# Kernel optimization log

Hardware: AMD Instinct MI355X
Metric: run time of the kernel (lower is better)

Reference implementation:

```python
import jax, jax.numpy as jnp
import numpy as np

N, E, IN, H, C, ED = 50000, 400000, 128, 8, 32, 16
NEG = 0.2   # LeakyReLU negative_slope
EPS = 1e-5  # LayerNorm eps


def _glorot(k, fan_in, fan_out, shape=None):
    lim = float(np.sqrt(6.0 / (fan_in + fan_out)))
    shape = (fan_in, fan_out) if shape is None else shape
    return jax.random.uniform(k, shape, jnp.float32, -lim, lim)


def setup_inputs() -> dict:
    key = jax.random.key(0)
    ks = jax.random.split(key, 16)
    x = jax.random.normal(ks[0], (N, IN), jnp.float32)
    src = jax.random.randint(ks[1], (E,), 0, N, jnp.int32)
    off = jax.random.randint(ks[2], (E,), 1, N, jnp.int32)
    dst = ((src + off) % N).astype(jnp.int32)  # guarantees no self loops
    edge_index = jnp.stack([src, dst])
    edge_attr = jax.random.normal(ks[3], (E, ED), jnp.float32) * 0.5
    d = {"x": x, "edge_index": edge_index, "edge_attr": edge_attr}
    i = 4
    for l, cin in [(1, IN), (2, C)]:
        d[f"Wl{l}"] = _glorot(ks[i], cin, H * C); i += 1
        d[f"bl{l}"] = jnp.zeros((H * C,), jnp.float32)
        d[f"Wr{l}"] = _glorot(ks[i], cin, H * C); i += 1
        d[f"br{l}"] = jnp.zeros((H * C,), jnp.float32)
        d[f"We{l}"] = _glorot(ks[i], ED, H * C); i += 1  # lin_edge, bias=False
        d[f"att{l}"] = _glorot(ks[i], H * C, 1, shape=(H, C)); i += 1
        d[f"bias{l}"] = jnp.zeros((C,), jnp.float32)
    d["ln_g"] = jnp.ones((C,), jnp.float32)
    d["ln_b"] = jnp.zeros((C,), jnp.float32)
    return d


def _seg_softmax(e, idx, n):
    # softmax over edges grouped by destination node (variable-degree neighborhoods)
    m = jax.ops.segment_max(e, idx, num_segments=n)
    p = jnp.exp(e - m[idx])
    s = jax.ops.segment_sum(p, idx, num_segments=n)
    return p / (s[idx] + 1e-16)


def _gat_layer(xx, src, dst, ea, Wl, bl, Wr, br, We, att, bias):
    n = xx.shape[0]
    xl = (xx @ Wl + bl).reshape(n, H, C)   # source transform (also the message)
    xr = (xx @ Wr + br).reshape(n, H, C)   # target transform
    ee = (ea @ We).reshape(-1, H, C)       # edge transform
    z = jax.nn.leaky_relu(xl[src] + xr[dst] + ee, NEG)      # [E', H, C]
    logits = jnp.einsum('ehc,hc->eh', z, att)               # [E', H]
    alpha = _seg_softmax(logits, dst, n)
    out = jax.ops.segment_sum(alpha[:, :, None] * xl[src], dst, num_segments=n)
    return out.mean(axis=1) + bias  # concat=False -> mean over heads


def _layernorm(xx, g, b):
    mu = jnp.mean(xx, -1, keepdims=True)
    var = jnp.mean((xx - mu) ** 2, -1, keepdims=True)
    return (xx - mu) * jax.lax.rsqrt(var + EPS) * g + b


def reference(x, edge_index, edge_attr, Wl1, bl1, Wr1, br1, We1, att1, bias1, ln_g, ln_b, Wl2, bl2, Wr2, br2, We2, att2, bias2):
    src, dst = edge_index[0], edge_index[1]
    # add_self_loops with fill_value='mean': self-loop attr = mean of incoming edge attrs
    deg = jax.ops.segment_sum(jnp.ones((E,), jnp.float32), dst, num_segments=N)
    loop_attr = jax.ops.segment_sum(edge_attr, dst, num_segments=N) / jnp.maximum(deg, 1.0)[:, None]
    ar = jnp.arange(N, dtype=src.dtype)
    src_f = jnp.concatenate([src, ar])
    dst_f = jnp.concatenate([dst, ar])
    ea_f = jnp.concatenate([edge_attr, loop_attr], axis=0)
    h = _gat_layer(x, src_f, dst_f, ea_f, Wl1, bl1, Wr1, br1, We1, att1, bias1)
    h = _layernorm(jax.nn.relu(h), ln_g, ln_b)
    h = _gat_layer(h, src_f, dst_f, ea_f, Wl2, bl2, Wr2, br2, We2, att2, bias2)
    return h
```

## Files before the change

### kernel.cpp

```cpp
#include <hip/hip_runtime.h>
#include <hip/hip_bf16.h>

#define N_NODES 50000
#define N_EDGES 400000
#define EP (N_EDGES + N_NODES)
#define IN_F 128
#define H_HEADS 8
#define C_CH 32
#define HC 256
#define ED_F 16
#define NEG_SLOPE 0.2f
#define LN_EPS 1e-5f
#define NB_SCAN ((N_NODES + 2047) / 2048)
#define NDBINS 1024
#define KF_NB 2048

typedef __hip_bfloat16 bf16;
typedef float v2f __attribute__((ext_vector_type(2)));
typedef short bf16x8 __attribute__((ext_vector_type(8)));
typedef float f32x4 __attribute__((ext_vector_type(4)));

__device__ __forceinline__ float bfu(unsigned short v){
    return __uint_as_float((unsigned int)v << 16);
}
__device__ __forceinline__ unsigned short f2b(float v){
    bf16 t = __float2bfloat16(v);
    return *reinterpret_cast<unsigned short*>(&t);
}

#define CASTX_NB 3125
#define W1_NB 128
#define W2_NB 32

__device__ __forceinline__ void prepW_body(const float* __restrict__ W,
                                           unsigned short* __restrict__ Wt,
                                           int K, int idx){
    if (idx >= 256 * K) return;
    int c = idx & 255, k = idx >> 8;
    Wt[(size_t)c * K + k] = f2b(W[idx]);
}

__global__ void k_prep(const float* __restrict__ x, unsigned short* __restrict__ xb,
                       const float* __restrict__ Wl1, unsigned short* __restrict__ Wt1l,
                       const float* __restrict__ Wr1, unsigned short* __restrict__ Wt1r,
                       const float* __restrict__ Wl2, unsigned short* __restrict__ Wt2l,
                       const float* __restrict__ Wr2, unsigned short* __restrict__ Wt2r){
    int b = blockIdx.x, t = threadIdx.x;
    if (b < CASTX_NB){
        int i = b * 256 + t;
        if (i >= N_NODES * IN_F / 8) return;
        const float4* p = reinterpret_cast<const float4*>(x + (size_t)i * 8);
        float4 v0 = p[0], v1 = p[1];
        unsigned short o[8] = {f2b(v0.x), f2b(v0.y), f2b(v0.z), f2b(v0.w),
                               f2b(v1.x), f2b(v1.y), f2b(v1.z), f2b(v1.w)};
        *reinterpret_cast<uint4*>(xb + (size_t)i * 8) = *reinterpret_cast<uint4*>(o);
    } else if (b < CASTX_NB + W1_NB){
        prepW_body(Wl1, Wt1l, IN_F, (b - CASTX_NB) * 256 + t);
    } else if (b < CASTX_NB + 2 * W1_NB){
        prepW_body(Wr1, Wt1r, IN_F, (b - CASTX_NB - W1_NB) * 256 + t);
    } else if (b < CASTX_NB + 2 * W1_NB + W2_NB){
        prepW_body(Wl2, Wt2l, C_CH, (b - CASTX_NB - 2 * W1_NB) * 256 + t);
    } else {
        prepW_body(Wr2, Wt2r, C_CH, (b - CASTX_NB - 2 * W1_NB - W2_NB) * 256 + t);
    }
}


__global__ void k_deg(const int* __restrict__ dstA, int* __restrict__ deg){
    int e = blockIdx.x * 256 + threadIdx.x;
    if (e < N_EDGES) atomicAdd(&deg[dstA[e]], 1);
}

__global__ void k_scanA(const int* __restrict__ deg, int* __restrict__ ptr,
                        int* __restrict__ bsum){
    __shared__ int wsum[4];
    int blk = blockIdx.x;
    int base0 = blk * 2048;
    int t = threadIdx.x, lane = t & 63, wv = t >> 6;
    int carry = 0;
    for (int c = 0; c < 8; ++c){
        int i = base0 + c * 256 + t;
        int v = (i < N_NODES) ? (deg[i] + 1) : 0;
        int x = v;
#pragma unroll
        for (int off = 1; off < 64; off <<= 1){
            int y = __shfl_up(x, off, 64);
            if (lane >= off) x += y;
        }
        if (lane == 63) wsum[wv] = x;
        __syncthreads();
        int pre = carry;
        for (int j = 0; j < wv; ++j) pre += wsum[j];
        if (i < N_NODES) ptr[i] = pre + x - v;
        int tot = wsum[0] + wsum[1] + wsum[2] + wsum[3];
        __syncthreads();
        carry += tot;
    }
    if (t == 0) bsum[blk] = carry;
}

__global__ void k_scanB(const int* __restrict__ bsum, int* __restrict__ boff){
    int t = threadIdx.x;
    int v = (t < NB_SCAN) ? bsum[t] : 0;
    int x = v;
#pragma unroll
    for (int off = 1; off < 64; off <<= 1){
        int y = __shfl_up(x, off, 64);
        if (t >= off) x += y;
    }
    if (t < NB_SCAN) boff[t] = x - v;
    if (t == 63) boff[NB_SCAN] = x;
}

__global__ void k_scanC(int* __restrict__ ptr, const int* __restrict__ boff){
    int i = blockIdx.x * 256 + threadIdx.x;
    if (i < N_NODES) ptr[i] += boff[i >> 11];
    else if (i == N_NODES) ptr[i] = boff[NB_SCAN];
}

__global__ void k_scatter(const int* __restrict__ dstA, const int* __restrict__ ptr,
                          int* __restrict__ cur, int* __restrict__ eid){
    int e = blockIdx.x * 256 + threadIdx.x;
    if (e >= EP) return;
    int n = (e < N_EDGES) ? dstA[e] : (e - N_EDGES);
    int p = ptr[n] + atomicAdd(&cur[n], 1);
    eid[p] = e;
}

__global__ void k_sort(const int* __restrict__ ptr, int* __restrict__ eid,
                       const int* __restrict__ srcA, int2* __restrict__ es){
    int n = blockIdx.x * 256 + threadIdx.x;
    if (n >= N_NODES) return;
    int b = ptr[n], t = ptr[n + 1];
    for (int i = b + 1; i < t; ++i){
        int v = eid[i]; int j = i - 1;
        while (j >= b && eid[j] > v){ eid[j + 1] = eid[j]; --j; }
        eid[j + 1] = v;
    }
    for (int i = b; i < t; ++i){
        int e = eid[i];
        es[i] = make_int2(e, (e < N_EDGES) ? srcA[e] : n);
    }
}

__global__ void k_loopattr(const int* __restrict__ ptr, const int* __restrict__ eid,
                           const float* __restrict__ ea, const int* __restrict__ deg,
                           float* __restrict__ la){
    int idx = blockIdx.x * 256 + threadIdx.x;
    if (idx >= N_NODES * ED_F) return;
    int n = idx >> 4, j = idx & 15;
    float s = 0.f;
    int b = ptr[n], t = ptr[n + 1];
    for (int i = b; i < t; ++i){
        int e = eid[i];
        if (e < N_EDGES) s += ea[(size_t)e * ED_F + j];
    }
    la[idx] = s / (float)max(deg[n], 1);
}

__global__ void k_hist(const int* __restrict__ ptr, int* __restrict__ hist){
    __shared__ int lh[NDBINS];
    int t = threadIdx.x;
    for (int i = t; i < NDBINS; i += 256) lh[i] = 0;
    __syncthreads();
    int n = blockIdx.x * 256 + t;
    if (n < N_NODES){
        int d = min(ptr[n + 1] - ptr[n], NDBINS - 1);
        atomicAdd(&lh[NDBINS - 1 - d], 1);
    }
    __syncthreads();
    for (int i = t; i < NDBINS; i += 256)
        if (lh[i]) atomicAdd(&hist[i], lh[i]);
}

__global__ void k_scanH(const int* __restrict__ hist, int* __restrict__ hoff){
    __shared__ int wsum[4];
    __shared__ int carry_s;
    int t = threadIdx.x, lane = t & 63, wv = t >> 6;
    if (t == 0) carry_s = 0;
    __syncthreads();
    for (int base = 0; base < NDBINS; base += 256){
        int i = base + t;
        int v = hist[i];
        int x = v;
#pragma unroll
        for (int off = 1; off < 64; off <<= 1){
            int y = __shfl_up(x, off, 64);
            if (lane >= off) x += y;
        }
        if (lane == 63) wsum[wv] = x;
        __syncthreads();
        int pre = carry_s;
        for (int j = 0; j < wv; ++j) pre += wsum[j];
        hoff[i] = pre + x - v;
        int tot = wsum[0] + wsum[1] + wsum[2] + wsum[3];
        __syncthreads();
        if (t == 0) carry_s += tot;
        __syncthreads();
    }
}

__global__ void k_place(const int* __restrict__ ptr, const int* __restrict__ hoff,
                        int* __restrict__ hcur, int* __restrict__ ord){
    __shared__ int lh[NDBINS];
    __shared__ int lbase[NDBINS];
    int t = threadIdx.x;
    for (int i = t; i < NDBINS; i += 256) lh[i] = 0;
    __syncthreads();
    int n = blockIdx.x * 256 + t;
    int b = -1, lr = 0;
    if (n < N_NODES){
        int d = min(ptr[n + 1] - ptr[n], NDBINS - 1);
        b = NDBINS - 1 - d;
        lr = atomicAdd(&lh[b], 1);
    }
    __syncthreads();
    for (int i = t; i < NDBINS; i += 256)
        if (lh[i]) lbase[i] = atomicAdd(&hcur[i], lh[i]);
    __syncthreads();
    if (n < N_NODES) ord[hoff[b] + lbase[b] + lr] = n;
}

template<int K>
__global__ __launch_bounds__(256)
void k_gemmM(const unsigned short* __restrict__ A,
             const unsigned short* __restrict__ Wtl, const float* __restrict__ bl,
             const unsigned short* __restrict__ Wtr, const float* __restrict__ br,
             bf16* __restrict__ xlh, unsigned short* __restrict__ xrh){
    const int cb = blockIdx.y;
    const unsigned short* Wt = (cb < 2) ? Wtl : Wtr;
    const float* bs = (cb < 2) ? bl : br;
    const int c0 = (cb & 1) * 128;
    const int r0 = blockIdx.x * 64;

    __shared__ unsigned short sA[64][40];
    __shared__ unsigned short sW[128][40];

    const int tid = threadIdx.x;
    const int lane = tid & 63;
    const int w = tid >> 6;

    f32x4 acc[8] = {};

    for (int kt = 0; kt < K; kt += 32){
        {
            int row = tid >> 2, kc = (tid & 3) * 8;
            int gr = r0 + row;
            uint4 v = make_uint4(0, 0, 0, 0);
            if (gr < N_NODES)
                v = *reinterpret_cast<const uint4*>(&A[(size_t)gr * K + kt + kc]);
            *reinterpret_cast<uint4*>(&sA[row][kc]) = v;
        }
        {
            int c = tid >> 1, kc = (tid & 1) * 16;
            const unsigned short* src = &Wt[(size_t)(c0 + c) * K + kt + kc];
            *reinterpret_cast<uint4*>(&sW[c][kc])     = *reinterpret_cast<const uint4*>(src);
            *reinterpret_cast<uint4*>(&sW[c][kc + 8]) = *reinterpret_cast<const uint4*>(src + 8);
        }
        __syncthreads();
        int kchunk = (lane >> 4) * 8;
        bf16x8 af = *reinterpret_cast<const bf16x8*>(&sA[w * 16 + (lane & 15)][kchunk]);
#pragma unroll
        for (int f = 0; f < 8; ++f){
            bf16x8 bfr = *reinterpret_cast<const bf16x8*>(&sW[f * 16 + (lane & 15)][kchunk]);
            acc[f] = __builtin_amdgcn_mfma_f32_16x16x32_bf16(af, bfr, acc[f], 0, 0, 0);
        }
        __syncthreads();
    }
    int colL = lane & 15;
    int rbase = (lane >> 4) * 4;
#pragma unroll
    for (int f = 0; f < 8; ++f){
        int col = c0 + f * 16 + colL;
        float bv = bs[col];
#pragma unroll
        for (int r = 0; r < 4; ++r){
            int gr = r0 + w * 16 + rbase + r;
            if (gr < N_NODES){
                float ov = acc[f][r] + bv;
                if (cb < 2) xlh[(size_t)gr * HC + col] = __float2bfloat16(ov);
                else        xrh[(size_t)gr * HC + col] = f2b(ov);
            }
        }
    }
}

template<int MODE>
__global__ __launch_bounds__(256)
__attribute__((amdgpu_waves_per_eu(3, 4)))
void k_fused(const bf16* __restrict__ xlh, const unsigned short* __restrict__ xrh,
             const float* __restrict__ ea, const float* __restrict__ la,
             const int2* __restrict__ es, const int* __restrict__ ptr,
             const int* __restrict__ ord,
             const float* __restrict__ We, const float* __restrict__ att,
             const float* __restrict__ bias, const float* __restrict__ lng,
             const float* __restrict__ lnb,
             unsigned short* __restrict__ h1b, float* __restrict__ outF){
    const int wv = threadIdx.x >> 6;
    const int lane = threadIdx.x & 63;
    const int c0 = lane * 4;
    const int k = lane & 7;

    v2f we2[ED_F][2];
#pragma unroll
    for (int j = 0; j < ED_F; ++j){
        float4 t4 = *reinterpret_cast<const float4*>(We + (size_t)j * HC + c0);
        we2[j][0] = v2f{t4.x, t4.y};
        we2[j][1] = v2f{t4.z, t4.w};
    }
    float4 at4 = *reinterpret_cast<const float4*>(att + c0);
    float attr[4] = {at4.x, at4.y, at4.z, at4.w};

#define EDGE_MLP(PK, AR, AK)                                              \
        {                                                                 \
            v2f z[2] = {AK[0] + xrv[0], AK[1] + xrv[1]};                  \
            _Pragma("unroll")                                             \
            for (int j4 = 0; j4 < 4; ++j4){                               \
                float4 e4 = *reinterpret_cast<const float4*>(AR + j4 * 4);\
                const float ej[4] = {e4.x, e4.y, e4.z, e4.w};             \
                _Pragma("unroll")                                         \
                for (int jj = 0; jj < 4; ++jj){                           \
                    int j = j4 * 4 + jj;                                  \
                    v2f ejv = {ej[jj], ej[jj]};                           \
                    z[0] += ejv * we2[j][0];                              \
                    z[1] += ejv * we2[j][1];                              \
                }                                                         \
            }                                                             \
            float zz0 = z[0].x, zz1 = z[0].y, zz2 = z[1].x, zz3 = z[1].y; \
            zz0 = (zz0 < 0.f) ? NEG_SLOPE * zz0 : zz0;                    \
            zz1 = (zz1 < 0.f) ? NEG_SLOPE * zz1 : zz1;                    \
            zz2 = (zz2 < 0.f) ? NEG_SLOPE * zz2 : zz2;                    \
            zz3 = (zz3 < 0.f) ? NEG_SLOPE * zz3 : zz3;                    \
            PK = zz0 * attr[0] + zz1 * attr[1] + zz2 * attr[2] + zz3 * attr[3]; \
        }

    const int nw = KF_NB * 4;
    for (int idx = blockIdx.x * 4 + wv; idx < N_NODES; idx += nw){
        int n = ord[idx];
        ushort4 xu = *reinterpret_cast<const ushort4*>(xrh + (size_t)n * HC + c0);
        v2f xrv[2] = {v2f{bfu(xu.x), bfu(xu.y)}, v2f{bfu(xu.z), bfu(xu.w)}};

        int b = ptr[n], tend = ptr[n + 1];
        float ssum = 0.f;
        v2f accv[2] = {v2f{0.f, 0.f}, v2f{0.f, 0.f}};

        int i = b;
        for (; i + 4 <= tend; i += 4){
            int2 q0 = es[i], q1 = es[i + 1], q2 = es[i + 2], q3 = es[i + 3];
            int e0 = __builtin_amdgcn_readfirstlane(q0.x);
            int s0 = __builtin_amdgcn_readfirstlane(q0.y);
            int e1 = __builtin_amdgcn_readfirstlane(q1.x);
            int s1 = __builtin_amdgcn_readfirstlane(q1.y);
            int e2 = __builtin_amdgcn_readfirstlane(q2.x);
            int s2 = __builtin_amdgcn_readfirstlane(q2.y);
            int e3 = __builtin_amdgcn_readfirstlane(q3.x);
            int s3 = __builtin_amdgcn_readfirstlane(q3.y);
            const float* ar0 = (e0 < N_EDGES) ? ea + (size_t)e0 * ED_F : la + (size_t)(e0 - N_EDGES) * ED_F;
            const float* ar1 = (e1 < N_EDGES) ? ea + (size_t)e1 * ED_F : la + (size_t)(e1 - N_EDGES) * ED_F;
            const float* ar2 = (e2 < N_EDGES) ? ea + (size_t)e2 * ED_F : la + (size_t)(e2 - N_EDGES) * ED_F;
            const float* ar3 = (e3 < N_EDGES) ? ea + (size_t)e3 * ED_F : la + (size_t)(e3 - N_EDGES) * ED_F;

            ushort4 u0 = *reinterpret_cast<const ushort4*>(xlh + (size_t)s0 * HC + c0);
            ushort4 u1 = *reinterpret_cast<const ushort4*>(xlh + (size_t)s1 * HC + c0);
            ushort4 u2 = *reinterpret_cast<const ushort4*>(xlh + (size_t)s2 * HC + c0);
            ushort4 u3 = *reinterpret_cast<const ushort4*>(xlh + (size_t)s3 * HC + c0);

            v2f a0[2] = {v2f{bfu(u0.x), bfu(u0.y)}, v2f{bfu(u0.z), bfu(u0.w)}};
            v2f a1[2] = {v2f{bfu(u1.x), bfu(u1.y)}, v2f{bfu(u1.z), bfu(u1.w)}};
            v2f a2[2] = {v2f{bfu(u2.x), bfu(u2.y)}, v2f{bfu(u2.z), bfu(u2.w)}};
            v2f a3[2] = {v2f{bfu(u3.x), bfu(u3.y)}, v2f{bfu(u3.z), bfu(u3.w)}};

            float p0, p1, p2, p3;
            EDGE_MLP(p0, ar0, a0)
            EDGE_MLP(p1, ar1, a1)
            EDGE_MLP(p2, ar2, a2)
            EDGE_MLP(p3, ar3, a3)

            p0 += __shfl_xor(p0, 1, 64); p1 += __shfl_xor(p1, 1, 64);
            p2 += __shfl_xor(p2, 1, 64); p3 += __shfl_xor(p3, 1, 64);
            p0 += __shfl_xor(p0, 2, 64); p1 += __shfl_xor(p1, 2, 64);
            p2 += __shfl_xor(p2, 2, 64); p3 += __shfl_xor(p3, 2, 64);
            p0 += __shfl_xor(p0, 4, 64); p1 += __shfl_xor(p1, 4, 64);
            p2 += __shfl_xor(p2, 4, 64); p3 += __shfl_xor(p3, 4, 64);

            float w0 = __expf(p0);
            float w1 = __expf(p1);
            float w2 = __expf(p2);
            float w3 = __expf(p3);
            ssum += w0 + w1 + w2 + w3;
            v2f w0v = {w0, w0}, w1v = {w1, w1}, w2v = {w2, w2}, w3v = {w3, w3};
#pragma unroll
            for (int q = 0; q < 2; ++q){
                accv[q] = accv[q] + w0v * a0[q] + w1v * a1[q] + w2v * a2[q] + w3v * a3[q];
            }
        }
        for (; i < tend; ++i){
            int2 q0 = es[i];
            int e0 = __builtin_amdgcn_readfirstlane(q0.x);
            int s0 = __builtin_amdgcn_readfirstlane(q0.y);
            const float* ar0 = (e0 < N_EDGES) ? ea + (size_t)e0 * ED_F : la + (size_t)(e0 - N_EDGES) * ED_F;
            ushort4 u0 = *reinterpret_cast<const ushort4*>(xlh + (size_t)s0 * HC + c0);
            v2f a0[2] = {v2f{bfu(u0.x), bfu(u0.y)}, v2f{bfu(u0.z), bfu(u0.w)}};
            float p0;
            EDGE_MLP(p0, ar0, a0)
            p0 += __shfl_xor(p0, 1, 64);
            p0 += __shfl_xor(p0, 2, 64);
            p0 += __shfl_xor(p0, 4, 64);
            float w0 = __expf(p0);
            ssum += w0;
            v2f w0v = {w0, w0};
            accv[0] = accv[0] + w0v * a0[0];
            accv[1] = accv[1] + w0v * a0[1];
        }

        float inv = 1.f / (ssum + 1e-16f);
        float acc[4] = {accv[0].x * inv, accv[0].y * inv, accv[1].x * inv, accv[1].y * inv};
#pragma unroll
        for (int q = 0; q < 4; ++q){
            acc[q] += __shfl_xor(acc[q], 8, 64);
            acc[q] += __shfl_xor(acc[q], 16, 64);
            acc[q] += __shfl_xor(acc[q], 32, 64);
        }
        float val[4];
#pragma unroll
        for (int q = 0; q < 4; ++q) val[q] = acc[q] * 0.125f + bias[k * 4 + q];

        if (MODE == 0){
            float r[4], s1 = 0.f, s2 = 0.f;
#pragma unroll
            for (int q = 0; q < 4; ++q){ r[q] = fmaxf(val[q], 0.f); s1 += r[q]; s2 += r[q] * r[q]; }
#pragma unroll
            for (int msk = 1; msk <= 4; msk <<= 1){
                s1 += __shfl_xor(s1, msk, 64);
                s2 += __shfl_xor(s2, msk, 64);
            }
            float mu = s1 * (1.f / 32.f);
            float var = s2 * (1.f / 32.f) - mu * mu;
            float rinv = rsqrtf(var + LN_EPS);
            if (lane < 8){
                unsigned short o[4];
#pragma unroll
                for (int q = 0; q < 4; ++q)
                    o[q] = f2b((r[q] - mu) * rinv * lng[k * 4 + q] + lnb[k * 4 + q]);
                *reinterpret_cast<ushort4*>(h1b + (size_t)n * C_CH + k * 4) =
                    *reinterpret_cast<ushort4*>(o);
            }
        } else {
            if (lane < 8){
                *reinterpret_cast<float4*>(outF + (size_t)n * C_CH + k * 4) =
                    make_float4(val[0], val[1], val[2], val[3]);
            }
        }
    }
#undef EDGE_MLP
}


extern "C" void kernel_launch(void* const* d_in, const int* in_sizes, int n_in,
                              void* d_out, int out_size, void* d_ws, size_t ws_size,
                              hipStream_t stream){
    const float* x    = (const float*)d_in[0];
    const int*   ei   = (const int*)d_in[1];
    const float* ea   = (const float*)d_in[2];
    const float* Wl1  = (const float*)d_in[3];
    const float* bl1  = (const float*)d_in[4];
    const float* Wr1  = (const float*)d_in[5];
    const float* br1  = (const float*)d_in[6];
    const float* We1  = (const float*)d_in[7];
    const float* att1 = (const float*)d_in[8];
    const float* bias1= (const float*)d_in[9];
    const float* Wl2  = (const float*)d_in[10];
    const float* bl2  = (const float*)d_in[11];
    const float* Wr2  = (const float*)d_in[12];
    const float* br2  = (const float*)d_in[13];
    const float* We2  = (const float*)d_in[14];
    const float* att2 = (const float*)d_in[15];
    const float* bias2= (const float*)d_in[16];
    const float* lng  = (const float*)d_in[17];
    const float* lnb  = (const float*)d_in[18];
    const int* srcA = ei;
    const int* dstA = ei + N_EDGES;

    char* w = (char*)d_ws;
    bf16*  xlh = (bf16*)w;                    w += (size_t)N_NODES * HC * 2;
    unsigned short* xrh = (unsigned short*)w; w += (size_t)N_NODES * HC * 2;
    unsigned short* xb  = (unsigned short*)w; w += (size_t)N_NODES * IN_F * 2;
    unsigned short* h1b = (unsigned short*)w; w += (size_t)N_NODES * C_CH * 2;
    float* la  = (float*)w;                   w += (size_t)N_NODES * ED_F * 4;
    unsigned short* Wt1l = (unsigned short*)w; w += (size_t)HC * IN_F * 2;
    unsigned short* Wt1r = (unsigned short*)w; w += (size_t)HC * IN_F * 2;
    unsigned short* Wt2l = (unsigned short*)w; w += (size_t)HC * C_CH * 2;
    unsigned short* Wt2r = (unsigned short*)w; w += (size_t)HC * C_CH * 2;
    int* deg   = (int*)w;   w += (size_t)N_NODES * 4;
    int* cur   = (int*)w;   w += (size_t)N_NODES * 4;
    int* hist  = (int*)w;   w += (size_t)NDBINS * 4;
    int* hcur  = (int*)w;   w += (size_t)NDBINS * 4;
    int* ptr   = (int*)w;   w += (size_t)(N_NODES + 1) * 4;
    int* eid   = (int*)w;   w += (size_t)EP * 4;
    int2* es   = (int2*)w;  w += (size_t)EP * 8;
    int* bsum  = (int*)w;   w += (size_t)(NB_SCAN + 1) * 4;
    int* boff  = (int*)w;   w += (size_t)(NB_SCAN + 1) * 4;
    int* hoff  = (int*)w;   w += (size_t)NDBINS * 4;
    int* ord   = (int*)w;   w += (size_t)N_NODES * 4;

    hipMemsetAsync(deg, 0, (size_t)(2 * N_NODES + 2 * NDBINS) * 4, stream);

    k_prep<<<CASTX_NB + 2 * W1_NB + 2 * W2_NB, 256, 0, stream>>>(
        x, xb, Wl1, Wt1l, Wr1, Wt1r, Wl2, Wt2l, Wr2, Wt2r);

    k_deg<<<(N_EDGES + 255) / 256, 256, 0, stream>>>(dstA, deg);
    k_scanA<<<NB_SCAN, 256, 0, stream>>>(deg, ptr, bsum);
    k_scanB<<<1, 64, 0, stream>>>(bsum, boff);
    k_scanC<<<(N_NODES + 256) / 256, 256, 0, stream>>>(ptr, boff);
    k_scatter<<<(EP + 255) / 256, 256, 0, stream>>>(dstA, ptr, cur, eid);
    k_sort<<<(N_NODES + 255) / 256, 256, 0, stream>>>(ptr, eid, srcA, es);
    k_loopattr<<<(N_NODES * ED_F + 255) / 256, 256, 0, stream>>>(ptr, eid, ea, deg, la);
    k_hist<<<(N_NODES + 255) / 256, 256, 0, stream>>>(ptr, hist);
    k_scanH<<<1, 256, 0, stream>>>(hist, hoff);
    k_place<<<(N_NODES + 255) / 256, 256, 0, stream>>>(ptr, hoff, hcur, ord);

    dim3 gg((N_NODES + 63) / 64, 4);
    k_gemmM<IN_F><<<gg, 256, 0, stream>>>(xb, Wt1l, bl1, Wt1r, br1, xlh, xrh);
    k_fused<0><<<KF_NB, 256, 0, stream>>>(xlh, xrh, ea, la, es, ptr, ord, We1, att1,
                                          bias1, lng, lnb, h1b, nullptr);
    k_gemmM<C_CH><<<gg, 256, 0, stream>>>(h1b, Wt2l, bl2, Wt2r, br2, xlh, xrh);
    k_fused<1><<<KF_NB, 256, 0, stream>>>(xlh, xrh, ea, la, es, ptr, ord, We2, att2,
                                          bias2, nullptr, nullptr, nullptr, (float*)d_out);
}
```

Baseline: 391.9 us.

## Store edge attributes and edge weights in fp16 and use packed dot2 for edge MLP

Edge attributes, the mean self-loop attributes and the edge-transform weights are converted to fp16 in the prep and loop-attr kernels. The fused attention kernel then computes the edge projection with fdot2 instructions on packed fp16 pairs instead of fp32 FMAs. This halves edge-attribute gather traffic and cuts edge-MLP ALU work and weight registers, which lets the occupancy hint rise from 3-4 to 4-8 waves per EU. In exchange it adds an extra cast pass over edge_attr each call and loses some precision in the edge term.

```diff
diff --git a/kernel.cpp b/kernel.cpp
--- a/kernel.cpp
+++ b/kernel.cpp
@@ -19,6 +19,7 @@
 typedef float v2f __attribute__((ext_vector_type(2)));
 typedef short bf16x8 __attribute__((ext_vector_type(8)));
 typedef float f32x4 __attribute__((ext_vector_type(4)));
+typedef _Float16 h2f __attribute__((ext_vector_type(2)));
 
 __device__ __forceinline__ float bfu(unsigned short v){
     return __uint_as_float((unsigned int)v << 16);
@@ -27,8 +28,12 @@
     bf16 t = __float2bfloat16(v);
     return *reinterpret_cast<unsigned short*>(&t);
 }
+__device__ __forceinline__ h2f u2h(unsigned int u){
+    union { unsigned int u; h2f h; } x; x.u = u; return x.h;
+}
 
 #define CASTX_NB 3125
+#define CASTE_NB 3125
 #define W1_NB 128
 #define W2_NB 32
 
@@ -41,10 +46,13 @@
 }
 
 __global__ void k_prep(const float* __restrict__ x, unsigned short* __restrict__ xb,
+                       const float* __restrict__ ea, _Float16* __restrict__ eah,
                        const float* __restrict__ Wl1, unsigned short* __restrict__ Wt1l,
                        const float* __restrict__ Wr1, unsigned short* __restrict__ Wt1r,
                        const float* __restrict__ Wl2, unsigned short* __restrict__ Wt2l,
-                       const float* __restrict__ Wr2, unsigned short* __restrict__ Wt2r){
+                       const float* __restrict__ Wr2, unsigned short* __restrict__ Wt2r,
+                       const float* __restrict__ We1, _Float16* __restrict__ weh1T,
+                       const float* __restrict__ We2, _Float16* __restrict__ weh2T){
     int b = blockIdx.x, t = threadIdx.x;
     if (b < CASTX_NB){
         int i = b * 256 + t;
@@ -54,14 +62,29 @@
         unsigned short o[8] = {f2b(v0.x), f2b(v0.y), f2b(v0.z), f2b(v0.w),
                                f2b(v1.x), f2b(v1.y), f2b(v1.z), f2b(v1.w)};
         *reinterpret_cast<uint4*>(xb + (size_t)i * 8) = *reinterpret_cast<uint4*>(o);
-    } else if (b < CASTX_NB + W1_NB){
-        prepW_body(Wl1, Wt1l, IN_F, (b - CASTX_NB) * 256 + t);
-    } else if (b < CASTX_NB + 2 * W1_NB){
-        prepW_body(Wr1, Wt1r, IN_F, (b - CASTX_NB - W1_NB) * 256 + t);
-    } else if (b < CASTX_NB + 2 * W1_NB + W2_NB){
-        prepW_body(Wl2, Wt2l, C_CH, (b - CASTX_NB - 2 * W1_NB) * 256 + t);
+    } else if (b < CASTX_NB + CASTE_NB){
+        int i = (b - CASTX_NB) * 256 + t;
+        const float4* p = reinterpret_cast<const float4*>(ea + (size_t)i * 8);
+        float4 v0 = p[0], v1 = p[1];
+        _Float16 o[8] = {(_Float16)v0.x, (_Float16)v0.y, (_Float16)v0.z, (_Float16)v0.w,
+                         (_Float16)v1.x, (_Float16)v1.y, (_Float16)v1.z, (_Float16)v1.w};
+        *reinterpret_cast<uint4*>(eah + (size_t)i * 8) = *reinterpret_cast<uint4*>(o);
+    } else if (b < CASTX_NB + CASTE_NB + W1_NB){
+        prepW_body(Wl1, Wt1l, IN_F, (b - CASTX_NB - CASTE_NB) * 256 + t);
+    } else if (b < CASTX_NB + CASTE_NB + 2 * W1_NB){
+        prepW_body(Wr1, Wt1r, IN_F, (b - CASTX_NB - CASTE_NB - W1_NB) * 256 + t);
+    } else if (b < CASTX_NB + CASTE_NB + 2 * W1_NB + W2_NB){
+        prepW_body(Wl2, Wt2l, C_CH, (b - CASTX_NB - CASTE_NB - 2 * W1_NB) * 256 + t);
+    } else if (b < CASTX_NB + CASTE_NB + 2 * W1_NB + 2 * W2_NB){
+        prepW_body(Wr2, Wt2r, C_CH, (b - CASTX_NB - CASTE_NB - 2 * W1_NB - W2_NB) * 256 + t);
+    } else if (b == CASTX_NB + CASTE_NB + 2 * W1_NB + 2 * W2_NB){
+#pragma unroll
+        for (int j = 0; j < ED_F; ++j)
+            weh1T[t * ED_F + j] = (_Float16)We1[j * HC + t];
     } else {
-        prepW_body(Wr2, Wt2r, C_CH, (b - CASTX_NB - 2 * W1_NB - W2_NB) * 256 + t);
+#pragma unroll
+        for (int j = 0; j < ED_F; ++j)
+            weh2T[t * ED_F + j] = (_Float16)We2[j * HC + t];
     }
 }
 
@@ -145,7 +168,7 @@
 
 __global__ void k_loopattr(const int* __restrict__ ptr, const int* __restrict__ eid,
                            const float* __restrict__ ea, const int* __restrict__ deg,
-                           float* __restrict__ la){
+                           _Float16* __restrict__ lah){
     int idx = blockIdx.x * 256 + threadIdx.x;
     if (idx >= N_NODES * ED_F) return;
     int n = idx >> 4, j = idx & 15;
@@ -155,7 +178,7 @@
         int e = eid[i];
         if (e < N_EDGES) s += ea[(size_t)e * ED_F + j];
     }
-    la[idx] = s / (float)max(deg[n], 1);
+    lah[idx] = (_Float16)(s / (float)max(deg[n], 1));
 }
 
 __global__ void k_hist(const int* __restrict__ ptr, int* __restrict__ hist){
@@ -287,12 +310,12 @@
 
 template<int MODE>
 __global__ __launch_bounds__(256)
-__attribute__((amdgpu_waves_per_eu(3, 4)))
+__attribute__((amdgpu_waves_per_eu(4, 8)))
 void k_fused(const bf16* __restrict__ xlh, const unsigned short* __restrict__ xrh,
-             const float* __restrict__ ea, const float* __restrict__ la,
+             const _Float16* __restrict__ eah, const _Float16* __restrict__ lah,
              const int2* __restrict__ es, const int* __restrict__ ptr,
              const int* __restrict__ ord,
-             const float* __restrict__ We, const float* __restrict__ att,
+             const _Float16* __restrict__ wehT, const float* __restrict__ att,
              const float* __restrict__ bias, const float* __restrict__ lng,
              const float* __restrict__ lnb,
              unsigned short* __restrict__ h1b, float* __restrict__ outF){
@@ -301,44 +324,43 @@
     const int c0 = lane * 4;
     const int k = lane & 7;
 
-    v2f we2[ED_F][2];
-#pragma unroll
-    for (int j = 0; j < ED_F; ++j){
-        float4 t4 = *reinterpret_cast<const float4*>(We + (size_t)j * HC + c0);
-        we2[j][0] = v2f{t4.x, t4.y};
-        we2[j][1] = v2f{t4.z, t4.w};
+    h2f wh[4][8];
+#pragma unroll
+    for (int c = 0; c < 4; ++c){
+        uint4 wa = *reinterpret_cast<const uint4*>(wehT + (size_t)(c0 + c) * ED_F);
+        uint4 wb = *reinterpret_cast<const uint4*>(wehT + (size_t)(c0 + c) * ED_F + 8);
+        wh[c][0] = u2h(wa.x); wh[c][1] = u2h(wa.y); wh[c][2] = u2h(wa.z); wh[c][3] = u2h(wa.w);
+        wh[c][4] = u2h(wb.x); wh[c][5] = u2h(wb.y); wh[c][6] = u2h(wb.z); wh[c][7] = u2h(wb.w);
     }
     float4 at4 = *reinterpret_cast<const float4*>(att + c0);
-    float attr[4] = {at4.x, at4.y, at4.z, at4.w};
-
-#define EDGE_MLP(PK, AR, AK)                                              \
+
+#define EDGE_MLP(PK, AR, U)                                               \
         {                                                                 \
-            v2f z[2] = {AK[0] + xrv[0], AK[1] + xrv[1]};                  \
+            uint4 ua = *reinterpret_cast<const uint4*>(AR);               \
+            uint4 ub = *reinterpret_cast<const uint4*>(AR + 8);           \
+            h2f eh_[8] = {u2h(ua.x), u2h(ua.y), u2h(ua.z), u2h(ua.w),     \
+                          u2h(ub.x), u2h(ub.y), u2h(ub.z), u2h(ub.w)};    \
+            float z0 = bfu(U.x) + xr0, z1 = bfu(U.y) + xr1;               \
+            float z2 = bfu(U.z) + xr2, z3 = bfu(U.w) + xr3;               \
             _Pragma("unroll")                                             \
-            for (int j4 = 0; j4 < 4; ++j4){                               \
-                float4 e4 = *reinterpret_cast<const float4*>(AR + j4 * 4);\
-                const float ej[4] = {e4.x, e4.y, e4.z, e4.w};             \
-                _Pragma("unroll")                                         \
-                for (int jj = 0; jj < 4; ++jj){                           \
-                    int j = j4 * 4 + jj;                                  \
-                    v2f ejv = {ej[jj], ej[jj]};                           \
-                    z[0] += ejv * we2[j][0];                              \
-                    z[1] += ejv * we2[j][1];                              \
-                }                                                         \
+            for (int j2 = 0; j2 < 8; ++j2){                               \
+                z0 = __builtin_amdgcn_fdot2(eh_[j2], wh[0][j2], z0, false);\
+                z1 = __builtin_amdgcn_fdot2(eh_[j2], wh[1][j2], z1, false);\
+                z2 = __builtin_amdgcn_fdot2(eh_[j2], wh[2][j2], z2, false);\
+                z3 = __builtin_amdgcn_fdot2(eh_[j2], wh[3][j2], z3, false);\
             }                                                             \
-            float zz0 = z[0].x, zz1 = z[0].y, zz2 = z[1].x, zz3 = z[1].y; \
-            zz0 = (zz0 < 0.f) ? NEG_SLOPE * zz0 : zz0;                    \
-            zz1 = (zz1 < 0.f) ? NEG_SLOPE * zz1 : zz1;                    \
-            zz2 = (zz2 < 0.f) ? NEG_SLOPE * zz2 : zz2;                    \
-            zz3 = (zz3 < 0.f) ? NEG_SLOPE * zz3 : zz3;                    \
-            PK = zz0 * attr[0] + zz1 * attr[1] + zz2 * attr[2] + zz3 * attr[3]; \
+            z0 = (z0 < 0.f) ? NEG_SLOPE * z0 : z0;                        \
+            z1 = (z1 < 0.f) ? NEG_SLOPE * z1 : z1;                        \
+            z2 = (z2 < 0.f) ? NEG_SLOPE * z2 : z2;                        \
+            z3 = (z3 < 0.f) ? NEG_SLOPE * z3 : z3;                        \
+            PK = z0 * at4.x + z1 * at4.y + z2 * at4.z + z3 * at4.w;       \
         }
 
     const int nw = KF_NB * 4;
     for (int idx = blockIdx.x * 4 + wv; idx < N_NODES; idx += nw){
         int n = ord[idx];
         ushort4 xu = *reinterpret_cast<const ushort4*>(xrh + (size_t)n * HC + c0);
-        v2f xrv[2] = {v2f{bfu(xu.x), bfu(xu.y)}, v2f{bfu(xu.z), bfu(xu.w)}};
+        float xr0 = bfu(xu.x), xr1 = bfu(xu.y), xr2 = bfu(xu.z), xr3 = bfu(xu.w);
 
         int b = ptr[n], tend = ptr[n + 1];
         float ssum = 0.f;
@@ -355,26 +377,21 @@
             int s2 = __builtin_amdgcn_readfirstlane(q2.y);
             int e3 = __builtin_amdgcn_readfirstlane(q3.x);
             int s3 = __builtin_amdgcn_readfirstlane(q3.y);
-            const float* ar0 = (e0 < N_EDGES) ? ea + (size_t)e0 * ED_F : la + (size_t)(e0 - N_EDGES) * ED_F;
-            const float* ar1 = (e1 < N_EDGES) ? ea + (size_t)e1 * ED_F : la + (size_t)(e1 - N_EDGES) * ED_F;
-            const float* ar2 = (e2 < N_EDGES) ? ea + (size_t)e2 * ED_F : la + (size_t)(e2 - N_EDGES) * ED_F;
-            const float* ar3 = (e3 < N_EDGES) ? ea + (size_t)e3 * ED_F : la + (size_t)(e3 - N_EDGES) * ED_F;
+            const _Float16* ar0 = (e0 < N_EDGES) ? eah + (size_t)e0 * ED_F : lah + (size_t)(e0 - N_EDGES) * ED_F;
+            const _Float16* ar1 = (e1 < N_EDGES) ? eah + (size_t)e1 * ED_F : lah + (size_t)(e1 - N_EDGES) * ED_F;
+            const _Float16* ar2 = (e2 < N_EDGES) ? eah + (size_t)e2 * ED_F : lah + (size_t)(e2 - N_EDGES) * ED_F;
+            const _Float16* ar3 = (e3 < N_EDGES) ? eah + (size_t)e3 * ED_F : lah + (size_t)(e3 - N_EDGES) * ED_F;
 
             ushort4 u0 = *reinterpret_cast<const ushort4*>(xlh + (size_t)s0 * HC + c0);
             ushort4 u1 = *reinterpret_cast<const ushort4*>(xlh + (size_t)s1 * HC + c0);
             ushort4 u2 = *reinterpret_cast<const ushort4*>(xlh + (size_t)s2 * HC + c0);
             ushort4 u3 = *reinterpret_cast<const ushort4*>(xlh + (size_t)s3 * HC + c0);
 
-            v2f a0[2] = {v2f{bfu(u0.x), bfu(u0.y)}, v2f{bfu(u0.z), bfu(u0.w)}};
-            v2f a1[2] = {v2f{bfu(u1.x), bfu(u1.y)}, v2f{bfu(u1.z), bfu(u1.w)}};
-            v2f a2[2] = {v2f{bfu(u2.x), bfu(u2.y)}, v2f{bfu(u2.z), bfu(u2.w)}};
-            v2f a3[2] = {v2f{bfu(u3.x), bfu(u3.y)}, v2f{bfu(u3.z), bfu(u3.w)}};
-
             float p0, p1, p2, p3;
-            EDGE_MLP(p0, ar0, a0)
-            EDGE_MLP(p1, ar1, a1)
-            EDGE_MLP(p2, ar2, a2)
-            EDGE_MLP(p3, ar3, a3)
+            EDGE_MLP(p0, ar0, u0)
+            EDGE_MLP(p1, ar1, u1)
+            EDGE_MLP(p2, ar2, u2)
+            EDGE_MLP(p3, ar3, u3)
 
             p0 += __shfl_xor(p0, 1, 64); p1 += __shfl_xor(p1, 1, 64);
             p2 += __shfl_xor(p2, 1, 64); p3 += __shfl_xor(p3, 1, 64);
@@ -389,28 +406,27 @@
             float w3 = __expf(p3);
             ssum += w0 + w1 + w2 + w3;
             v2f w0v = {w0, w0}, w1v = {w1, w1}, w2v = {w2, w2}, w3v = {w3, w3};
-#pragma unroll
-            for (int q = 0; q < 2; ++q){
-                accv[q] = accv[q] + w0v * a0[q] + w1v * a1[q] + w2v * a2[q] + w3v * a3[q];
-            }
+            accv[0] += w0v * v2f{bfu(u0.x), bfu(u0.y)} + w1v * v2f{bfu(u1.x), bfu(u1.y)}
+                     + w2v * v2f{bfu(u2.x), bfu(u2.y)} + w3v * v2f{bfu(u3.x), bfu(u3.y)};
+            accv[1] += w0v * v2f{bfu(u0.z), bfu(u0.w)} + w1v * v2f{bfu(u1.z), bfu(u1.w)}
+                     + w2v * v2f{bfu(u2.z), bfu(u2.w)} + w3v * v2f{bfu(u3.z), bfu(u3.w)};
         }
         for (; i < tend; ++i){
             int2 q0 = es[i];
             int e0 = __builtin_amdgcn_readfirstlane(q0.x);
             int s0 = __builtin_amdgcn_readfirstlane(q0.y);
-            const float* ar0 = (e0 < N_EDGES) ? ea + (size_t)e0 * ED_F : la + (size_t)(e0 - N_EDGES) * ED_F;
+            const _Float16* ar0 = (e0 < N_EDGES) ? eah + (size_t)e0 * ED_F : lah + (size_t)(e0 - N_EDGES) * ED_F;
             ushort4 u0 = *reinterpret_cast<const ushort4*>(xlh + (size_t)s0 * HC + c0);
-            v2f a0[2] = {v2f{bfu(u0.x), bfu(u0.y)}, v2f{bfu(u0.z), bfu(u0.w)}};
             float p0;
-            EDGE_MLP(p0, ar0, a0)
+            EDGE_MLP(p0, ar0, u0)
             p0 += __shfl_xor(p0, 1, 64);
             p0 += __shfl_xor(p0, 2, 64);
             p0 += __shfl_xor(p0, 4, 64);
             float w0 = __expf(p0);
             ssum += w0;
             v2f w0v = {w0, w0};
-            accv[0] = accv[0] + w0v * a0[0];
-            accv[1] = accv[1] + w0v * a0[1];
+            accv[0] += w0v * v2f{bfu(u0.x), bfu(u0.y)};
+            accv[1] += w0v * v2f{bfu(u0.z), bfu(u0.w)};
         }
 
         float inv = 1.f / (ssum + 1e-16f);
@@ -486,7 +502,10 @@
     unsigned short* xrh = (unsigned short*)w; w += (size_t)N_NODES * HC * 2;
     unsigned short* xb  = (unsigned short*)w; w += (size_t)N_NODES * IN_F * 2;
     unsigned short* h1b = (unsigned short*)w; w += (size_t)N_NODES * C_CH * 2;
-    float* la  = (float*)w;                   w += (size_t)N_NODES * ED_F * 4;
+    _Float16* eah = (_Float16*)w;             w += (size_t)N_EDGES * ED_F * 2;
+    _Float16* lah = (_Float16*)w;             w += (size_t)N_NODES * ED_F * 2;
+    _Float16* weh1T = (_Float16*)w;           w += (size_t)HC * ED_F * 2;
+    _Float16* weh2T = (_Float16*)w;           w += (size_t)HC * ED_F * 2;
     unsigned short* Wt1l = (unsigned short*)w; w += (size_t)HC * IN_F * 2;
     unsigned short* Wt1r = (unsigned short*)w; w += (size_t)HC * IN_F * 2;
     unsigned short* Wt2l = (unsigned short*)w; w += (size_t)HC * C_CH * 2;
@@ -505,8 +524,9 @@
 
     hipMemsetAsync(deg, 0, (size_t)(2 * N_NODES + 2 * NDBINS) * 4, stream);
 
-    k_prep<<<CASTX_NB + 2 * W1_NB + 2 * W2_NB, 256, 0, stream>>>(
-        x, xb, Wl1, Wt1l, Wr1, Wt1r, Wl2, Wt2l, Wr2, Wt2r);
+    k_prep<<<CASTX_NB + CASTE_NB + 2 * W1_NB + 2 * W2_NB + 2, 256, 0, stream>>>(
+        x, xb, ea, eah, Wl1, Wt1l, Wr1, Wt1r, Wl2, Wt2l, Wr2, Wt2r,
+        We1, weh1T, We2, weh2T);
 
     k_deg<<<(N_EDGES + 255) / 256, 256, 0, stream>>>(dstA, deg);
     k_scanA<<<NB_SCAN, 256, 0, stream>>>(deg, ptr, bsum);
@@ -514,16 +534,16 @@
     k_scanC<<<(N_NODES + 256) / 256, 256, 0, stream>>>(ptr, boff);
     k_scatter<<<(EP + 255) / 256, 256, 0, stream>>>(dstA, ptr, cur, eid);
     k_sort<<<(N_NODES + 255) / 256, 256, 0, stream>>>(ptr, eid, srcA, es);
-    k_loopattr<<<(N_NODES * ED_F + 255) / 256, 256, 0, stream>>>(ptr, eid, ea, deg, la);
+    k_loopattr<<<(N_NODES * ED_F + 255) / 256, 256, 0, stream>>>(ptr, eid, ea, deg, lah);
     k_hist<<<(N_NODES + 255) / 256, 256, 0, stream>>>(ptr, hist);
     k_scanH<<<1, 256, 0, stream>>>(hist, hoff);
     k_place<<<(N_NODES + 255) / 256, 256, 0, stream>>>(ptr, hoff, hcur, ord);
 
     dim3 gg((N_NODES + 63) / 64, 4);
     k_gemmM<IN_F><<<gg, 256, 0, stream>>>(xb, Wt1l, bl1, Wt1r, br1, xlh, xrh);
-    k_fused<0><<<KF_NB, 256, 0, stream>>>(xlh, xrh, ea, la, es, ptr, ord, We1, att1,
+    k_fused<0><<<KF_NB, 256, 0, stream>>>(xlh, xrh, eah, lah, es, ptr, ord, weh1T, att1,
                                           bias1, lng, lnb, h1b, nullptr);
     k_gemmM<C_CH><<<gg, 256, 0, stream>>>(h1b, Wt2l, bl2, Wt2r, br2, xlh, xrh);
-    k_fused<1><<<KF_NB, 256, 0, stream>>>(xlh, xrh, ea, la, es, ptr, ord, We2, att2,
+    k_fused<1><<<KF_NB, 256, 0, stream>>>(xlh, xrh, eah, lah, es, ptr, ord, weh2T, att2,
                                           bias2, nullptr, nullptr, nullptr, (float*)d_out);
 }
```

New measurement: 362.5 us. -7.5%, faster.
